# Kernel tuning notes

Hardware: AMD Instinct MI355X
Metric: run time of the kernel (lower is better)

Reference implementation:

```python
import jax, jax.numpy as jnp
import numpy as np

H, S, B, R, IN, NN, OP = 512, 256, 32, 16, 4, 16, 6
NEG = -1.0e12


def setup_inputs() -> dict:
    key = jax.random.key(0)
    ks = jax.random.split(key, 40)
    f32 = jnp.float32
    inp = {}
    inp["node_emb"] = jax.random.normal(ks[0], (B, 1, H), f32)
    inp["left"] = jax.random.normal(ks[1], (B, 1, H), f32)
    inp["encoder_outputs"] = jax.random.normal(ks[2], (S, B, H), f32)
    inp["num_pades"] = jax.random.normal(ks[3], (B, NN, H), f32)
    inp["formula_scores"] = jax.random.normal(ks[4], (R, H), f32)
    inp["has_left"] = jax.random.bernoulli(ks[5], 0.5, (B,))
    lengths = jax.random.randint(ks[6], (B,), S // 2, S + 1)
    inp["seq_mask"] = jnp.arange(S)[None, :] >= lengths[:, None]
    nlen = jax.random.randint(ks[7], (B,), (IN + NN) // 2, IN + NN + 1)
    inp["mask_nums"] = jnp.arange(IN + NN)[None, :] >= nlen[:, None]
    sc = 0.04  # init scale for weights
    def w(i, shape):
        return jax.random.normal(ks[i], shape, f32) * sc
    inp["embedding_weight"] = jax.random.normal(ks[8], (1, IN, H), f32)
    inp["Wcl"] = w(9, (H, H));    inp["bcl"] = jnp.zeros((H,), f32)
    inp["Wclg"] = w(10, (H, H));  inp["bclg"] = jnp.zeros((H,), f32)
    inp["Wcr"] = w(11, (2 * H, H));  inp["bcr"] = jnp.zeros((H,), f32)
    inp["Wcrg"] = w(12, (2 * H, H)); inp["bcrg"] = jnp.zeros((H,), f32)
    inp["Wops"] = w(13, (2 * H, OP)); inp["bops"] = jnp.zeros((OP,), f32)
    inp["Wattn"] = w(14, (2 * H, H)); inp["battn"] = jnp.zeros((H,), f32)
    inp["wattn_s"] = w(15, (H,));     inp["battn_s"] = jnp.zeros((), f32)
    inp["Wfattn"] = w(16, (2 * H, H)); inp["bfattn"] = jnp.zeros((H,), f32)
    inp["wfattn_s"] = w(17, (H,));     inp["bfattn_s"] = jnp.zeros((), f32)
    inp["Wscore"] = w(18, (3 * H, H)); inp["bscore"] = jnp.zeros((H,), f32)
    inp["wscore_s"] = w(19, (H,))  # Score.score has no bias
    inp["Wfp1"] = w(20, (H, H));   inp["bfp1"] = jnp.zeros((H,), f32)
    inp["Wfp2"] = w(21, (H,));     inp["bfp2"] = jnp.zeros((), f32)
    return inp


def _forward(node_emb, left, has_left, encoder_outputs, num_pades, seq_mask,
             mask_nums, formula_scores, embedding_weight, Wcl, bcl, Wclg, bclg,
             Wcr, bcr, Wcrg, bcrg, Wops, bops, Wattn, battn, wattn_s, battn_s,
             Wfattn, bfattn, wfattn_s, bfattn_s, Wscore, bscore, wscore_s,
             Wfp1, bfp1, Wfp2, bfp2):
    # gated left/right node update (dropout = identity, eval mode)
    c = node_emb                                            # [B,1,H]
    lc = jnp.concatenate([left, c], axis=-1)                # [B,1,2H]
    out_l = jnp.tanh(c @ Wcl + bcl) * jax.nn.sigmoid(c @ Wclg + bclg)
    out_r = jnp.tanh(lc @ Wcr + bcr) * jax.nn.sigmoid(lc @ Wcrg + bcrg)
    current_node = jnp.where(has_left[:, None, None], out_r, out_l)  # [B,1,H]
    # TreeAttn(current_node, encoder_outputs): additive attention over S
    Wh, We = Wattn[:H], Wattn[H:]
    feat = jnp.tanh(current_node[:, 0][None] @ Wh + encoder_outputs @ We + battn)  # [S,B,H]
    en = (feat @ wattn_s + battn_s).T                       # [B,S]
    en = jnp.where(seq_mask, NEG, en)
    current_attn = jax.nn.softmax(en, axis=1)[:, None, :]   # [B,1,S]
    eo_b = jnp.transpose(encoder_outputs, (1, 0, 2))        # [B,S,H]
    current_context = current_attn @ eo_b                   # [B,1,H]
    # embedding table = learned constants + numbers from the problem
    emb_w = jnp.concatenate(
        [jnp.broadcast_to(embedding_weight, (node_emb.shape[0], IN, H)), num_pades], axis=1)  # [B,IN+NN,H]
    leaf_input = jnp.concatenate([current_node, current_context], axis=2)[:, 0]  # [B,2H]
    # FormulaAttn: additive attention of each formula over all tokens
    Wfe, Wff = Wfattn[:H], Wfattn[H:]
    ffeat = jnp.tanh(encoder_outputs[None] @ Wfe
                     + (formula_scores @ Wff)[:, None, None, :] + bfattn)  # [R,S,B,H]
    fen = jnp.transpose(ffeat @ wfattn_s + bfattn_s, (2, 0, 1))            # [B,R,S]
    fen = jnp.where(seq_mask[:, None, :], NEG, fen)
    formulas_attn = jax.nn.softmax(fen, axis=-1)            # [B,R,S]
    formulas_context = (formulas_attn + 0.2 * current_attn) @ eo_b         # [B,R,H]
    formula_feat = jnp.tanh(formulas_context @ Wfp1 + bfp1)
    formula_prob = jax.nn.softmax(formula_feat @ Wfp2 + bfp2, axis=-1)     # [B,R]
    # Score over candidate number embeddings
    N = IN + NN
    hid = jnp.broadcast_to(leaf_input[:, None, :], (leaf_input.shape[0], N, 2 * H))
    ein = jnp.concatenate([hid, emb_w], axis=-1)            # [B,N,3H]
    ns = jnp.tanh(ein @ Wscore + bscore) @ wscore_s         # [B,N]
    num_score = jnp.where(mask_nums, NEG, ns)
    op = leaf_input @ Wops + bops                           # [B,OP]
    return (num_score, op, current_node, current_context, emb_w, formula_prob)


def reference(node_emb, left, has_left, encoder_outputs, num_pades, seq_mask,
              mask_nums, formula_scores, embedding_weight, Wcl, bcl, Wclg, bclg,
              Wcr, bcr, Wcrg, bcrg, Wops, bops, Wattn, battn, wattn_s, battn_s,
              Wfattn, bfattn, wfattn_s, bfattn_s, Wscore, bscore, wscore_s,
              Wfp1, bfp1, Wfp2, bfp2):
    return _forward(node_emb, left, has_left, encoder_outputs, num_pades,
                    seq_mask, mask_nums, formula_scores, embedding_weight,
                    Wcl, bcl, Wclg, bclg, Wcr, bcr, Wcrg, bcrg, Wops, bops,
                    Wattn, battn, wattn_s, battn_s, Wfattn, bfattn, wfattn_s,
                    bfattn_s, Wscore, bscore, wscore_s, Wfp1, bfp1, Wfp2, bfp2)
```

## Files before the change

kernel.cpp:

```cpp
#include <hip/hip_runtime.h>
#include <hip/hip_bf16.h>
#include <stdint.h>

#define H 512
#define S 256
#define B 32
#define R 16
#define NEG -1000000000000.0f

typedef unsigned short u16;
typedef short short8 __attribute__((ext_vector_type(8)));
typedef float f32x4 __attribute__((ext_vector_type(4)));

__device__ __forceinline__ float bf2f(u16 u) {
  unsigned int v = ((unsigned int)u) << 16;
  float f; __builtin_memcpy(&f, &v, 4); return f;
}
__device__ __forceinline__ u16 f2u(float x) {
  __hip_bfloat16 h = __float2bfloat16(x);
  u16 u; __builtin_memcpy(&u, &h, 2); return u;
}
__device__ __forceinline__ float ftanh(float x) {
  float e = __expf(2.f * x);
  return 1.f - 2.f * __builtin_amdgcn_rcpf(e + 1.f);
}
__device__ __forceinline__ float ptanh(float x) {
  float xc = fminf(4.f, fmaxf(-4.f, x));
  float x2 = xc * xc;
  float num = xc * (945.f + x2 * (105.f + x2));
  float den = 945.f + x2 * (420.f + 15.f * x2);
  return num * __builtin_amdgcn_rcpf(den);
}
__device__ __forceinline__ float fsig(float x) {
  return __builtin_amdgcn_rcpf(1.f + __expf(-x));
}
__device__ __forceinline__ void gload16(const void* g, void* l) {
  __builtin_amdgcn_global_load_lds(
      (const __attribute__((address_space(1))) unsigned int*)g,
      (__attribute__((address_space(3))) unsigned int*)l, 16, 0, 0);
}

__device__ __forceinline__ void trans_tile(const float* __restrict__ src, int nb, int k0,
                                           u16* __restrict__ dst, int n0, int Krows,
                                           float (*tile)[65], int t) {
  #pragma unroll
  for (int it = 0; it < 16; ++it) {
    int f = it * 256 + t; int r = f >> 6, c = f & 63;
    tile[r][c] = src[(size_t)(k0 + r) * 512 + nb + c];
  }
  __syncthreads();
  #pragma unroll
  for (int it = 0; it < 16; ++it) {
    int f = it * 256 + t; int r = f >> 6, c = f & 63;
    dst[(size_t)(n0 + r) * Krows + k0 + c] = f2u(tile[c][r]);
  }
}

__global__ __launch_bounds__(256) void k_prep1(
    const float* __restrict__ enc, u16* __restrict__ encb,
    const float* __restrict__ Wattn, const float* __restrict__ Wfattn, u16* __restrict__ Wt,
    const float* __restrict__ Wscore, u16* __restrict__ Wt2a, u16* __restrict__ Wt2b,
    const float* __restrict__ Wfp1, u16* __restrict__ Wt3,
    u16* __restrict__ Wt4,
    const float* __restrict__ node_emb, const float* __restrict__ left,
    const int* __restrict__ has_left,
    const float* __restrict__ Wcl, const float* __restrict__ Wclg,
    const float* __restrict__ Wcr, const float* __restrict__ Wcrg,
    float* __restrict__ gp1, float* __restrict__ gp2,
    const float* __restrict__ emb_w, const float* __restrict__ num_pades,
    float* __restrict__ out_embw, u16* __restrict__ embb, u16* __restrict__ leafb) {
  __shared__ float tile[64][65];
  __shared__ float x[128];
  int id = blockIdx.x, t = threadIdx.x;
  if (id < 2048) {
    int i = (id * 256 + t) * 8;
    float4 a = *(const float4*)(enc + i);
    float4 b = *(const float4*)(enc + i + 4);
    short8 o;
    o[0] = (short)f2u(a.x); o[1] = (short)f2u(a.y); o[2] = (short)f2u(a.z); o[3] = (short)f2u(a.w);
    o[4] = (short)f2u(b.x); o[5] = (short)f2u(b.y); o[6] = (short)f2u(b.z); o[7] = (short)f2u(b.w);
    *(short8*)(encb + i) = o;
  } else if (id < 2176) {
    int f = id - 2048; int gx = f & 15, gy = f >> 4;
    int n0 = gx * 64, k0 = gy * 64;
    const float* src = (n0 < 512) ? (Wattn + 512 * 512) : Wfattn;
    int nb = (n0 < 512) ? n0 : n0 - 512;
    trans_tile(src, nb, k0, Wt, n0, 512, tile, t);
  } else if (id < 2240) {
    int f = id - 2176; int gx = f & 7, gy = f >> 3;
    trans_tile(Wscore + 1024 * 512, gx * 64, gy * 64, Wt2a, gx * 64, 512, tile, t);
  } else if (id < 2368) {
    int f = id - 2240; int gx = f & 7, gy = f >> 3;
    trans_tile(Wscore, gx * 64, gy * 64, Wt2b, gx * 64, 1024, tile, t);
  } else if (id < 2432) {
    int f = id - 2368; int gx = f & 7, gy = f >> 3;
    trans_tile(Wfp1, gx * 64, gy * 64, Wt3, gx * 64, 512, tile, t);
  } else if (id < 2560) {
    int f = id - 2432; int gx = f & 15, gy = f >> 4;
    int n0 = gx * 64, k0 = gy * 64;
    const float* src = (n0 < 512) ? Wattn : (Wfattn + 512 * 512);
    int nb = (n0 < 512) ? n0 : n0 - 512;
    trans_tile(src, nb, k0, Wt4, n0, 512, tile, t);
  } else if (id < 2816) {
    int f = id - 2560;
    int b = f >> 3, kc = f & 7;
    int hl = has_left[b];
    int k0 = kc * 128;
    float* o1 = gp1 + ((size_t)b * 8 + kc) * 512;
    float* o2 = gp2 + ((size_t)b * 8 + kc) * 512;
    if (!hl && kc >= 4) { o1[t] = 0.f; o1[t + 256] = 0.f; o2[t] = 0.f; o2[t + 256] = 0.f; return; }
    if (t < 128) {
      int k = k0 + t;
      x[t] = hl ? (k < 512 ? left[b * 512 + k] : node_emb[b * 512 + k - 512])
                : node_emb[b * 512 + k];
    }
    __syncthreads();
    const float* W1 = hl ? Wcr : Wcl;
    const float* W2 = hl ? Wcrg : Wclg;
    float a1 = 0.f, a2 = 0.f, a3 = 0.f, a4 = 0.f;
    for (int kk = 0; kk < 128; ++kk) {
      float xv = x[kk];
      const float* w1r = W1 + (size_t)(k0 + kk) * 512;
      const float* w2r = W2 + (size_t)(k0 + kk) * 512;
      a1 += xv * w1r[t]; a2 += xv * w1r[t + 256];
      a3 += xv * w2r[t]; a4 += xv * w2r[t + 256];
    }
    o1[t] = a1; o1[t + 256] = a2; o2[t] = a3; o2[t + 256] = a4;
  } else if (id < 3136) {
    int f = id - 2816;
    #pragma unroll
    for (int rr = 0; rr < 2; ++rr) {
      int row = f * 2 + rr;
      int n = row % 20, b = row / 20;
      #pragma unroll
      for (int i = 0; i < 2; ++i) {
        int h = t + 256 * i;
        float v = (n < 4) ? emb_w[n * 512 + h] : num_pades[((size_t)b * 16 + n - 4) * 512 + h];
        out_embw[(size_t)row * 512 + h] = v;
        embb[(size_t)row * 512 + h] = f2u(v);
      }
    }
  } else {
    int f = id - 3136;
    int base = 32 * 1024 + (f * 256 + t) * 16;
    short8 z8 = {0,0,0,0,0,0,0,0};
    *(short8*)(leafb + base) = z8;
    *(short8*)(leafb + base + 8) = z8;
  }
}

template <int FM, int FN>
__device__ __forceinline__ void gemm_body(
    const u16* __restrict__ A, const u16* __restrict__ Bt,
    u16* __restrict__ C16, float* __restrict__ C32,
    int lda, int ldb, int ldc, int ksteps,
    int bm, int bn, int kbase, long zoff,
    u16* As, u16* Bs) {
  constexpr int BM = FM * 32, BN = FN * 32;
  const int tid = threadIdx.x;
  const int lane = tid & 63;
  const int wid = tid >> 6;
  const int wr = (wid >> 1) * (FM * 16);
  const int wc = (wid & 1) * (FN * 16);
  f32x4 acc[FM][FN];
  #pragma unroll
  for (int m = 0; m < FM; ++m)
    #pragma unroll
    for (int n = 0; n < FN; ++n)
      #pragma unroll
      for (int q = 0; q < 4; ++q) acc[m][n][q] = 0.f;

  const int kb = (lane >> 4) * 8;
  const int rr = lane & 15;
  for (int ks = 0; ks < ksteps; ++ks) {
    int k0 = kbase + ks * 32;
    #pragma unroll
    for (int it = 0; it < BM / 64; ++it) {
      int c = it * 256 + tid;
      gload16(A + (size_t)(bm + (c >> 2)) * lda + k0 + (c & 3) * 8, As + c * 8);
    }
    #pragma unroll
    for (int it = 0; it < BN / 64; ++it) {
      int c = it * 256 + tid;
      gload16(Bt + (size_t)(bn + (c >> 2)) * ldb + k0 + (c & 3) * 8, Bs + c * 8);
    }
    __syncthreads();
    short8 af[FM], bf[FN];
    #pragma unroll
    for (int m = 0; m < FM; ++m)
      af[m] = *(const short8*)(As + (wr + m * 16 + rr) * 32 + kb);
    #pragma unroll
    for (int n = 0; n < FN; ++n)
      bf[n] = *(const short8*)(Bs + (wc + n * 16 + rr) * 32 + kb);
    #pragma unroll
    for (int m = 0; m < FM; ++m)
      #pragma unroll
      for (int n = 0; n < FN; ++n)
        acc[m][n] = __builtin_amdgcn_mfma_f32_16x16x32_bf16(af[m], bf[n], acc[m][n], 0, 0, 0);
    __syncthreads();
  }
  int r0 = (lane >> 4) * 4, cc = lane & 15;
  #pragma unroll
  for (int m = 0; m < FM; ++m)
    #pragma unroll
    for (int n = 0; n < FN; ++n)
      #pragma unroll
      for (int q = 0; q < 4; ++q) {
        long row = bm + wr + m * 16 + r0 + q;
        long col = bn + wc + n * 16 + cc;
        if (C16) C16[zoff + row * ldc + col] = f2u(acc[m][n][q]);
        else     C32[zoff + row * ldc + col] = acc[m][n][q];
      }
}

__global__ __launch_bounds__(256) void k_g1(
    const u16* __restrict__ encb, const u16* __restrict__ Wt, u16* __restrict__ EW,
    const u16* __restrict__ cnfs, const u16* __restrict__ Wt4, float* __restrict__ CWFW) {
  __shared__ u16 As[128 * 32];
  __shared__ u16 Bs[128 * 32];
  int x = blockIdx.x, y = blockIdx.y;
  if (x < 64)
    gemm_body<4, 4>(encb, Wt, EW, nullptr, 512, 512, 1024, 16, x * 128, y * 128, 0, 0, As, Bs);
  else
    gemm_body<4, 4>(cnfs, Wt4, nullptr, CWFW, 512, 512, 1024, 16, 0, y * 128, 0, 0, As, Bs);
}

__global__ __launch_bounds__(256) void k_tt(
    const u16* __restrict__ embb, const u16* __restrict__ Wt2a, float* __restrict__ Tep,
    const u16* __restrict__ leafb, const u16* __restrict__ Wt2b, float* __restrict__ Tlp,
    const u16* __restrict__ fctxb, const u16* __restrict__ Wt3, float* __restrict__ T3p) {
  __shared__ u16 As[64 * 32];
  __shared__ u16 Bs[64 * 32];
  int q = blockIdx.x;
  if (q < 320) {
    int x = q % 10, y = (q / 10) % 8, z = q / 80;
    gemm_body<2, 2>(embb, Wt2a, nullptr, Tep, 512, 512, 512, 4,
                    x * 64, y * 64, z * 4 * 32, (long)z * 327680, As, Bs);
  } else if (q < 352) {
    int q2 = q - 320; int y = q2 % 8, z = q2 / 8;
    gemm_body<2, 2>(leafb, Wt2b, nullptr, Tlp, 1024, 1024, 512, 8,
                    0, y * 64, z * 8 * 32, (long)z * 32768, As, Bs);
  } else {
    int q2 = q - 352;
    int x = q2 % 8, y = (q2 / 8) % 8, z = q2 / 64;
    gemm_body<2, 2>(fctxb, Wt3, nullptr, T3p, 512, 512, 512, 4,
                    x * 64, y * 64, z * 4 * 32, (long)z * 262144, As, Bs);
  }
}

__global__ __launch_bounds__(256) void k_p2(
    const float* __restrict__ gp1, const float* __restrict__ gp2,
    const int* __restrict__ has_left,
    const float* __restrict__ bcl, const float* __restrict__ bclg,
    const float* __restrict__ bcr, const float* __restrict__ bcrg,
    const float* __restrict__ fs,
    float* __restrict__ cur_node, float* __restrict__ out_cn, u16* __restrict__ cnfs) {
  int id = blockIdx.x, t = threadIdx.x;
  if (id < 32) {
    int b = id, hl = has_left[b];
    #pragma unroll
    for (int i = 0; i < 2; ++i) {
      int h = t + 256 * i;
      float s1 = 0.f, s2 = 0.f;
      #pragma unroll
      for (int c = 0; c < 8; ++c) {
        s1 += gp1[((size_t)b * 8 + c) * 512 + h];
        s2 += gp2[((size_t)b * 8 + c) * 512 + h];
      }
      float v = ftanh(s1 + (hl ? bcr[h] : bcl[h])) * fsig(s2 + (hl ? bcrg[h] : bclg[h]));
      cur_node[b * 512 + h] = v;
      out_cn[b * 512 + h] = v;
      cnfs[b * 512 + h] = f2u(v);
    }
  } else if (id < 48) {
    int r = id - 32;
    #pragma unroll
    for (int i = 0; i < 2; ++i) {
      int h = t + 256 * i;
      cnfs[id * 512 + h] = f2u(fs[r * 512 + h]);
    }
  } else {
    #pragma unroll
    for (int i = 0; i < 2; ++i) cnfs[id * 512 + t + 256 * i] = 0;
  }
}

__global__ __launch_bounds__(256) void k_enfen(
    const u16* __restrict__ EW, const float* __restrict__ CWFW,
    const float* __restrict__ battn, const float* __restrict__ bfattn,
    const float* __restrict__ wattn_s, const float* __restrict__ battn_s,
    const float* __restrict__ wfattn_s, const float* __restrict__ bfattn_s,
    const int* __restrict__ seq_mask, float* __restrict__ en, float* __restrict__ fen) {
  __shared__ float sFW[16 * 512];
  __shared__ float swf[512], swa[512], scw[512];
  int bid = blockIdx.x;
  int b = bid >> 6;
  int s0 = (bid & 63) * 4;
  int t = threadIdx.x;
  #pragma unroll
  for (int q = 0; q < 32; ++q) {
    int flat = q * 256 + t;
    int r = flat >> 9, h = flat & 511;
    sFW[flat] = CWFW[(size_t)(32 + r) * 1024 + 512 + h] + bfattn[h];
  }
  swf[t] = wfattn_s[t]; swf[256 + t] = wfattn_s[256 + t];
  swa[t] = wattn_s[t];  swa[256 + t] = wattn_s[256 + t];
  scw[t] = CWFW[(size_t)b * 1024 + t] + battn[t];
  scw[256 + t] = CWFW[(size_t)b * 1024 + 256 + t] + battn[256 + t];
  __syncthreads();
  int w = t >> 6, lane = t & 63;
  int s = s0 + w;
  int msk = seq_mask[b * 256 + s];
  if (msk) {
    if (lane == 0) {
      en[b * 256 + s] = NEG;
      for (int r = 0; r < 16; ++r) fen[((size_t)b * 16 + r) * 256 + s] = NEG;
    }
    return;
  }
  const u16* ew = EW + (size_t)(s * 32 + b) * 1024;
  float ewf[8], wfv[8];
  float accE = 0.f;
  #pragma unroll
  for (int i = 0; i < 8; ++i) {
    int h = lane + 64 * i;
    accE += ptanh(scw[h] + bf2f(ew[h])) * swa[h];
    ewf[i] = bf2f(ew[512 + h]);
    wfv[i] = swf[h];
  }
  for (int o = 32; o >= 1; o >>= 1) accE += __shfl_down(accE, o);
  if (lane == 0) en[b * 256 + s] = accE + battn_s[0];
  for (int r = 0; r < 16; ++r) {
    float a = 0.f;
    #pragma unroll
    for (int i = 0; i < 8; ++i) {
      int h = lane + 64 * i;
      a += ptanh(sFW[r * 512 + h] + ewf[i]) * wfv[i];
    }
    for (int o = 32; o >= 1; o >>= 1) a += __shfl_down(a, o);
    if (lane == 0) fen[((size_t)b * 16 + r) * 256 + s] = a + bfattn_s[0];
  }
}

__global__ __launch_bounds__(512) void k_ctxall(
    const float* __restrict__ en, const float* __restrict__ fen,
    const u16* __restrict__ encb, const float* __restrict__ cur_node,
    float* __restrict__ out_ctx, float* __restrict__ leaf, u16* __restrict__ fctxb,
    u16* __restrict__ leafb) {
  int br = blockIdx.x;
  int b = br / 9, k = br % 9;
  int t = threadIdx.x;
  __shared__ float red[512];
  __shared__ float sa0[256], sa1[256];
  float xe = (t < 256) ? en[b * 256 + t] : NEG;
  red[t] = xe; __syncthreads();
  for (int o = 256; o > 0; o >>= 1) { if (t < o) red[t] = fmaxf(red[t], red[t + o]); __syncthreads(); }
  float m = red[0]; __syncthreads();
  float ee = (t < 256) ? __expf(xe - m) : 0.f;
  red[t] = ee; __syncthreads();
  for (int o = 256; o > 0; o >>= 1) { if (t < o) red[t] += red[t + o]; __syncthreads(); }
  float attn_v = ee / red[0];
  __syncthreads();
  if (k < 8) {
    #pragma unroll
    for (int p = 0; p < 2; ++p) {
      int j = k + p * 8;
      float xf = (t < 256) ? fen[((size_t)b * 16 + j) * 256 + t] : NEG;
      red[t] = xf; __syncthreads();
      for (int o = 256; o > 0; o >>= 1) { if (t < o) red[t] = fmaxf(red[t], red[t + o]); __syncthreads(); }
      float mf = red[0]; __syncthreads();
      float ef = (t < 256) ? __expf(xf - mf) : 0.f;
      red[t] = ef; __syncthreads();
      for (int o = 256; o > 0; o >>= 1) { if (t < o) red[t] += red[t + o]; __syncthreads(); }
      float coef = ef / red[0] + 0.2f * attn_v;
      __syncthreads();
      if (t < 256) { if (p == 0) sa0[t] = coef; else sa1[t] = coef; }
    }
    __syncthreads();
    int h = t;
    float acc0 = 0.f, acc1 = 0.f;
    #pragma unroll 8
    for (int s = 0; s < 256; ++s) {
      float ev = bf2f(encb[((size_t)s * 32 + b) * 512 + h]);
      acc0 += sa0[s] * ev;
      acc1 += sa1[s] * ev;
    }
    fctxb[((size_t)b * 16 + k) * 512 + h] = f2u(acc0);
    fctxb[((size_t)b * 16 + k + 8) * 512 + h] = f2u(acc1);
  } else {
    if (t < 256) sa0[t] = attn_v;
    __syncthreads();
    int h = t;
    float acc = 0.f;
    #pragma unroll 8
    for (int s = 0; s < 256; ++s)
      acc += sa0[s] * bf2f(encb[((size_t)s * 32 + b) * 512 + h]);
    float cn = cur_node[b * 512 + h];
    out_ctx[b * 512 + h] = acc;
    leaf[b * 1024 + 512 + h] = acc;
    leaf[b * 1024 + h] = cn;
    leafb[b * 1024 + h] = f2u(cn);
    leafb[b * 1024 + 512 + h] = f2u(acc);
  }
}

__global__ __launch_bounds__(256) void k_epi(
    const float* __restrict__ Tep, const float* __restrict__ Tlp,
    const float* __restrict__ bscore,
    const float* __restrict__ wscore_s, const int* __restrict__ mask_nums,
    float* __restrict__ out_ns,
    const float* __restrict__ T3p, const float* __restrict__ bfp1,
    const float* __restrict__ Wfp2, const float* __restrict__ bfp2,
    float* __restrict__ out_fp,
    const float* __restrict__ leaf, const float* __restrict__ Wops,
    const float* __restrict__ bops, float* __restrict__ out_op) {
  int id = blockIdx.x, t = threadIdx.x;
  int w = t >> 6, lane = t & 63;
  __shared__ float red[16];
  if (id < 640) {
    int row = id;
    int b = row / 20;
    float acc = 0.f;
    #pragma unroll
    for (int i = 0; i < 2; ++i) {
      int h = t + 256 * i;
      float tv = bscore[h];
      #pragma unroll
      for (int z = 0; z < 4; ++z) tv += Tep[(size_t)z * 327680 + (size_t)row * 512 + h];
      #pragma unroll
      for (int z = 0; z < 4; ++z) tv += Tlp[(size_t)z * 32768 + (size_t)b * 512 + h];
      acc += ftanh(tv) * wscore_s[h];
    }
    for (int o = 32; o >= 1; o >>= 1) acc += __shfl_down(acc, o);
    if (lane == 0) red[w] = acc;
    __syncthreads();
    if (t == 0) out_ns[row] = mask_nums[row] ? NEG : (red[0] + red[1] + red[2] + red[3]);
  } else if (id < 672) {
    int b = id - 640;
    #pragma unroll
    for (int j2 = 0; j2 < 4; ++j2) {
      int j = w * 4 + j2;
      int row = b * 16 + j;
      float acc = 0.f;
      #pragma unroll
      for (int i = 0; i < 8; ++i) {
        int h = lane + 64 * i;
        float v = bfp1[h];
        #pragma unroll
        for (int z = 0; z < 4; ++z) v += T3p[(size_t)z * 262144 + (size_t)row * 512 + h];
        acc += ftanh(v) * Wfp2[h];
      }
      for (int o = 32; o >= 1; o >>= 1) acc += __shfl_down(acc, o);
      if (lane == 0) red[j] = acc + bfp2[0];
    }
    __syncthreads();
    if (t < 16) {
      float xx = red[t];
      float mm = xx;
      for (int o = 8; o >= 1; o >>= 1) mm = fmaxf(mm, __shfl_xor(mm, o, 16));
      float e = __expf(xx - mm);
      float s2 = e;
      for (int o = 8; o >= 1; o >>= 1) s2 += __shfl_xor(s2, o, 16);
      out_fp[b * 16 + t] = e / s2;
    }
  } else {
    int f = id - 672; int o = f % 6, b = f / 6;
    float acc = 0.f;
    #pragma unroll
    for (int i = 0; i < 4; ++i) {
      int k = t + 256 * i;
      acc += leaf[b * 1024 + k] * Wops[(size_t)k * 6 + o];
    }
    for (int off = 32; off >= 1; off >>= 1) acc += __shfl_down(acc, off);
    if (lane == 0) red[w] = acc;
    __syncthreads();
    if (t == 0) out_op[b * 6 + o] = red[0] + red[1] + red[2] + red[3] + bops[o];
  }
}

extern "C" void kernel_launch(void* const* d_in, const int* in_sizes, int n_in,
                              void* d_out, int out_size, void* d_ws, size_t ws_size,
                              hipStream_t stream) {
  const float* node_emb  = (const float*)d_in[0];
  const float* left      = (const float*)d_in[1];
  const float* enc       = (const float*)d_in[2];
  const float* num_pades = (const float*)d_in[3];
  const float* fs        = (const float*)d_in[4];
  const int*   has_left  = (const int*)d_in[5];
  const int*   seq_mask  = (const int*)d_in[6];
  const int*   mask_nums = (const int*)d_in[7];
  const float* emb_w     = (const float*)d_in[8];
  const float* Wcl  = (const float*)d_in[9];
  const float* bcl  = (const float*)d_in[10];
  const float* Wclg = (const float*)d_in[11];
  const float* bclg = (const float*)d_in[12];
  const float* Wcr  = (const float*)d_in[13];
  const float* bcr  = (const float*)d_in[14];
  const float* Wcrg = (const float*)d_in[15];
  const float* bcrg = (const float*)d_in[16];
  const float* Wops = (const float*)d_in[17];
  const float* bops = (const float*)d_in[18];
  const float* Wattn   = (const float*)d_in[19];
  const float* battn   = (const float*)d_in[20];
  const float* wattn_s = (const float*)d_in[21];
  const float* battn_s = (const float*)d_in[22];
  const float* Wfattn   = (const float*)d_in[23];
  const float* bfattn   = (const float*)d_in[24];
  const float* wfattn_s = (const float*)d_in[25];
  const float* bfattn_s = (const float*)d_in[26];
  const float* Wscore   = (const float*)d_in[27];
  const float* bscore   = (const float*)d_in[28];
  const float* wscore_s = (const float*)d_in[29];
  const float* Wfp1 = (const float*)d_in[30];
  const float* bfp1 = (const float*)d_in[31];
  const float* Wfp2 = (const float*)d_in[32];
  const float* bfp2 = (const float*)d_in[33];

  float* out = (float*)d_out;
  float* out_ns   = out + 0;
  float* out_op   = out + 640;
  float* out_cn   = out + 832;
  float* out_ctx  = out + 17216;
  float* out_embw = out + 33600;
  float* out_fp   = out + 361280;

  uint8_t* wsb = (uint8_t*)d_ws;
  u16*   encb = (u16*)(wsb + 0);
  u16*   Wt   = (u16*)(wsb + 8388608);
  u16*   Wt2a = (u16*)(wsb + 9437184);
  u16*   Wt2b = (u16*)(wsb + 9961472);
  u16*   Wt3  = (u16*)(wsb + 11010048);
  u16*   Wt4  = (u16*)(wsb + 11534336);
  u16*   EW   = (u16*)(wsb + 12582912);
  u16*   embb = (u16*)(wsb + 29360128);
  u16*   leafb= (u16*)(wsb + 30015488);
  u16*   cnfs = (u16*)(wsb + 30146560);
  float* CWFW = (float*)(wsb + 30277632);
  float* Tep  = (float*)(wsb + 30801920);
  float* Tlp  = (float*)(wsb + 36044800);
  float* T3p  = (float*)(wsb + 36569088);
  float* fb   = (float*)(wsb + 40763392);
  float* cur_node = fb + 0;
  float* en   = fb + 16384;
  float* fen  = fb + 24576;
  float* leaf = fb + 155648;
  u16*   fctxb= (u16*)(fb + 188416);
  float* gp1  = fb + 319488;
  float* gp2  = fb + 450560;

  k_prep1<<<3144, 256, 0, stream>>>(enc, encb, Wattn, Wfattn, Wt, Wscore, Wt2a, Wt2b,
                                    Wfp1, Wt3, Wt4,
                                    node_emb, left, has_left, Wcl, Wclg, Wcr, Wcrg,
                                    gp1, gp2, emb_w, num_pades, out_embw, embb, leafb);
  k_p2<<<128, 256, 0, stream>>>(gp1, gp2, has_left, bcl, bclg, bcr, bcrg, fs,
                                cur_node, out_cn, cnfs);
  k_g1<<<dim3(65, 8), 256, 0, stream>>>(encb, Wt, EW, cnfs, Wt4, CWFW);
  k_enfen<<<2048, 256, 0, stream>>>(EW, CWFW, battn, bfattn, wattn_s, battn_s,
                                    wfattn_s, bfattn_s, seq_mask, en, fen);
  k_ctxall<<<288, 512, 0, stream>>>(en, fen, encb, cur_node, out_ctx, leaf, fctxb, leafb);
  k_tt<<<608, 256, 0, stream>>>(embb, Wt2a, Tep, leafb, Wt2b, Tlp, fctxb, Wt3, T3p);
  k_epi<<<864, 256, 0, stream>>>(Tep, Tlp, bscore, wscore_s, mask_nums, out_ns,
                                 T3p, bfp1, Wfp2, bfp2, out_fp,
                                 leaf, Wops, bops, out_op);
}
```

Before: 110.9 us.

## Rebalance work across kernels: move emb GEMM earlier, ops head earlier, batch enfen rows

The embedding-times-Wscore GEMM depends only on prep outputs, so it moves from the late k_tt launch into k_g1, where it runs alongside the encoder GEMM. The ops linear head moves from k_epi into k_tt, which shortens the critical path of the last kernels. k_enfen now has each wave process two sequence positions, which halves the block count and spreads the 16x512 shared-memory staging over more work. The trade-off is a mix of 64-tile and 128-tile GEMM blocks sharing one launch with the larger LDS footprint, which could lower occupancy for the small tiles.

```diff
diff --git a/kernel.cpp b/kernel.cpp
--- a/kernel.cpp
+++ b/kernel.cpp
@@ -215,36 +215,56 @@
 
 __global__ __launch_bounds__(256) void k_g1(
     const u16* __restrict__ encb, const u16* __restrict__ Wt, u16* __restrict__ EW,
-    const u16* __restrict__ cnfs, const u16* __restrict__ Wt4, float* __restrict__ CWFW) {
+    const u16* __restrict__ cnfs, const u16* __restrict__ Wt4, float* __restrict__ CWFW,
+    const u16* __restrict__ embb, const u16* __restrict__ Wt2a, float* __restrict__ Tep) {
   __shared__ u16 As[128 * 32];
   __shared__ u16 Bs[128 * 32];
-  int x = blockIdx.x, y = blockIdx.y;
-  if (x < 64)
+  int q = blockIdx.x;
+  if (q < 512) {
+    int x = q & 63, y = q >> 6;
     gemm_body<4, 4>(encb, Wt, EW, nullptr, 512, 512, 1024, 16, x * 128, y * 128, 0, 0, As, Bs);
-  else
+  } else if (q < 520) {
+    int y = q - 512;
     gemm_body<4, 4>(cnfs, Wt4, nullptr, CWFW, 512, 512, 1024, 16, 0, y * 128, 0, 0, As, Bs);
+  } else {
+    int q2 = q - 520;
+    int x = q2 % 10, y = (q2 / 10) % 8, z = q2 / 80;
+    gemm_body<2, 2>(embb, Wt2a, nullptr, Tep, 512, 512, 512, 4,
+                    x * 64, y * 64, z * 4 * 32, (long)z * 327680, As, Bs);
+  }
 }
 
 __global__ __launch_bounds__(256) void k_tt(
-    const u16* __restrict__ embb, const u16* __restrict__ Wt2a, float* __restrict__ Tep,
     const u16* __restrict__ leafb, const u16* __restrict__ Wt2b, float* __restrict__ Tlp,
-    const u16* __restrict__ fctxb, const u16* __restrict__ Wt3, float* __restrict__ T3p) {
+    const u16* __restrict__ fctxb, const u16* __restrict__ Wt3, float* __restrict__ T3p,
+    const float* __restrict__ leaf, const float* __restrict__ Wops,
+    const float* __restrict__ bops, float* __restrict__ out_op) {
   __shared__ u16 As[64 * 32];
   __shared__ u16 Bs[64 * 32];
+  __shared__ float red[4];
   int q = blockIdx.x;
-  if (q < 320) {
-    int x = q % 10, y = (q / 10) % 8, z = q / 80;
-    gemm_body<2, 2>(embb, Wt2a, nullptr, Tep, 512, 512, 512, 4,
-                    x * 64, y * 64, z * 4 * 32, (long)z * 327680, As, Bs);
-  } else if (q < 352) {
-    int q2 = q - 320; int y = q2 % 8, z = q2 / 8;
+  if (q < 32) {
+    int y = q % 8, z = q / 8;
     gemm_body<2, 2>(leafb, Wt2b, nullptr, Tlp, 1024, 1024, 512, 8,
                     0, y * 64, z * 8 * 32, (long)z * 32768, As, Bs);
-  } else {
-    int q2 = q - 352;
+  } else if (q < 288) {
+    int q2 = q - 32;
     int x = q2 % 8, y = (q2 / 8) % 8, z = q2 / 64;
     gemm_body<2, 2>(fctxb, Wt3, nullptr, T3p, 512, 512, 512, 4,
                     x * 64, y * 64, z * 4 * 32, (long)z * 262144, As, Bs);
+  } else {
+    int f = q - 288; int o = f % 6, b = f / 6;
+    int t = threadIdx.x, w = t >> 6, lane = t & 63;
+    float acc = 0.f;
+    #pragma unroll
+    for (int i = 0; i < 4; ++i) {
+      int k = t + 256 * i;
+      acc += leaf[b * 1024 + k] * Wops[(size_t)k * 6 + o];
+    }
+    for (int off = 32; off >= 1; off >>= 1) acc += __shfl_down(acc, off);
+    if (lane == 0) red[w] = acc;
+    __syncthreads();
+    if (t == 0) out_op[b * 6 + o] = red[0] + red[1] + red[2] + red[3] + bops[o];
   }
 }
 
@@ -294,8 +314,8 @@
   __shared__ float sFW[16 * 512];
   __shared__ float swf[512], swa[512], scw[512];
   int bid = blockIdx.x;
-  int b = bid >> 6;
-  int s0 = (bid & 63) * 4;
+  int b = bid >> 5;
+  int s0 = (bid & 31) * 8;
   int t = threadIdx.x;
   #pragma unroll
   for (int q = 0; q < 32; ++q) {
@@ -309,36 +329,44 @@
   scw[256 + t] = CWFW[(size_t)b * 1024 + 256 + t] + battn[256 + t];
   __syncthreads();
   int w = t >> 6, lane = t & 63;
-  int s = s0 + w;
-  int msk = seq_mask[b * 256 + s];
-  if (msk) {
-    if (lane == 0) {
-      en[b * 256 + s] = NEG;
-      for (int r = 0; r < 16; ++r) fen[((size_t)b * 16 + r) * 256 + s] = NEG;
-    }
-    return;
-  }
-  const u16* ew = EW + (size_t)(s * 32 + b) * 1024;
-  float ewf[8], wfv[8];
-  float accE = 0.f;
+  float wav[8], wfv[8], cwv[8];
   #pragma unroll
   for (int i = 0; i < 8; ++i) {
     int h = lane + 64 * i;
-    accE += ptanh(scw[h] + bf2f(ew[h])) * swa[h];
-    ewf[i] = bf2f(ew[512 + h]);
-    wfv[i] = swf[h];
-  }
-  for (int o = 32; o >= 1; o >>= 1) accE += __shfl_down(accE, o);
-  if (lane == 0) en[b * 256 + s] = accE + battn_s[0];
-  for (int r = 0; r < 16; ++r) {
-    float a = 0.f;
+    wav[i] = swa[h]; wfv[i] = swf[h]; cwv[i] = scw[h];
+  }
+  #pragma unroll
+  for (int si = 0; si < 2; ++si) {
+    int s = s0 + w * 2 + si;
+    int msk = seq_mask[b * 256 + s];
+    if (msk) {
+      if (lane == 0) {
+        en[b * 256 + s] = NEG;
+        for (int r = 0; r < 16; ++r) fen[((size_t)b * 16 + r) * 256 + s] = NEG;
+      }
+      continue;
+    }
+    const u16* ew = EW + (size_t)(s * 32 + b) * 1024;
+    float ewf[8];
+    float accE = 0.f;
     #pragma unroll
     for (int i = 0; i < 8; ++i) {
       int h = lane + 64 * i;
-      a += ptanh(sFW[r * 512 + h] + ewf[i]) * wfv[i];
-    }
-    for (int o = 32; o >= 1; o >>= 1) a += __shfl_down(a, o);
-    if (lane == 0) fen[((size_t)b * 16 + r) * 256 + s] = a + bfattn_s[0];
+      accE += ptanh(cwv[i] + bf2f(ew[h])) * wav[i];
+      ewf[i] = bf2f(ew[512 + h]);
+    }
+    for (int o = 32; o >= 1; o >>= 1) accE += __shfl_down(accE, o);
+    if (lane == 0) en[b * 256 + s] = accE + battn_s[0];
+    for (int r = 0; r < 16; ++r) {
+      float a = 0.f;
+      #pragma unroll
+      for (int i = 0; i < 8; ++i) {
+        int h = lane + 64 * i;
+        a += ptanh(sFW[r * 512 + h] + ewf[i]) * wfv[i];
+      }
+      for (int o = 32; o >= 1; o >>= 1) a += __shfl_down(a, o);
+      if (lane == 0) fen[((size_t)b * 16 + r) * 256 + s] = a + bfattn_s[0];
+    }
   }
 }
 
@@ -411,9 +439,7 @@
     float* __restrict__ out_ns,
     const float* __restrict__ T3p, const float* __restrict__ bfp1,
     const float* __restrict__ Wfp2, const float* __restrict__ bfp2,
-    float* __restrict__ out_fp,
-    const float* __restrict__ leaf, const float* __restrict__ Wops,
-    const float* __restrict__ bops, float* __restrict__ out_op) {
+    float* __restrict__ out_fp) {
   int id = blockIdx.x, t = threadIdx.x;
   int w = t >> 6, lane = t & 63;
   __shared__ float red[16];
@@ -435,7 +461,7 @@
     if (lane == 0) red[w] = acc;
     __syncthreads();
     if (t == 0) out_ns[row] = mask_nums[row] ? NEG : (red[0] + red[1] + red[2] + red[3]);
-  } else if (id < 672) {
+  } else {
     int b = id - 640;
     #pragma unroll
     for (int j2 = 0; j2 < 4; ++j2) {
@@ -463,18 +489,6 @@
       for (int o = 8; o >= 1; o >>= 1) s2 += __shfl_xor(s2, o, 16);
       out_fp[b * 16 + t] = e / s2;
     }
-  } else {
-    int f = id - 672; int o = f % 6, b = f / 6;
-    float acc = 0.f;
-    #pragma unroll
-    for (int i = 0; i < 4; ++i) {
-      int k = t + 256 * i;
-      acc += leaf[b * 1024 + k] * Wops[(size_t)k * 6 + o];
-    }
-    for (int off = 32; off >= 1; off >>= 1) acc += __shfl_down(acc, off);
-    if (lane == 0) red[w] = acc;
-    __syncthreads();
-    if (t == 0) out_op[b * 6 + o] = red[0] + red[1] + red[2] + red[3] + bops[o];
   }
 }
 
@@ -554,12 +568,12 @@
                                     gp1, gp2, emb_w, num_pades, out_embw, embb, leafb);
   k_p2<<<128, 256, 0, stream>>>(gp1, gp2, has_left, bcl, bclg, bcr, bcrg, fs,
                                 cur_node, out_cn, cnfs);
-  k_g1<<<dim3(65, 8), 256, 0, stream>>>(encb, Wt, EW, cnfs, Wt4, CWFW);
-  k_enfen<<<2048, 256, 0, stream>>>(EW, CWFW, battn, bfattn, wattn_s, battn_s,
+  k_g1<<<840, 256, 0, stream>>>(encb, Wt, EW, cnfs, Wt4, CWFW, embb, Wt2a, Tep);
+  k_enfen<<<1024, 256, 0, stream>>>(EW, CWFW, battn, bfattn, wattn_s, battn_s,
                                     wfattn_s, bfattn_s, seq_mask, en, fen);
   k_ctxall<<<288, 512, 0, stream>>>(en, fen, encb, cur_node, out_ctx, leaf, fctxb, leafb);
-  k_tt<<<608, 256, 0, stream>>>(embb, Wt2a, Tep, leafb, Wt2b, Tlp, fctxb, Wt3, T3p);
-  k_epi<<<864, 256, 0, stream>>>(Tep, Tlp, bscore, wscore_s, mask_nums, out_ns,
-                                 T3p, bfp1, Wfp2, bfp2, out_fp,
-                                 leaf, Wops, bops, out_op);
-}
+  k_tt<<<480, 256, 0, stream>>>(leafb, Wt2b, Tlp, fctxb, Wt3, T3p,
+                                leaf, Wops, bops, out_op);
+  k_epi<<<672, 256, 0, stream>>>(Tep, Tlp, bscore, wscore_s, mask_nums, out_ns,
+                                 T3p, bfp1, Wfp2, bfp2, out_fp);
+}
```

Result: faster. 104.8 us (-5.4%).
